# Performance work log

Hardware: AMD Instinct MI355X
Metric: run time of the kernel (lower is better)

The kernel has to match this reference:

```python
import jax, jax.numpy as jnp
import numpy as np

NUM_CODEBOOKS = 2
CODEBOOK_SIZE = 256
OUT_GROUP = 1
IN_GROUP = 8
IN_FEATURES = 4096
OUT_FEATURES = 11008


def setup_inputs() -> dict:
    key = jax.random.key(0)
    k1, k2, k3, k4, k5 = jax.random.split(key, 5)
    num_out_groups = OUT_FEATURES // OUT_GROUP
    num_in_groups = IN_FEATURES // IN_GROUP
    x = jax.random.normal(k1, (4, 2048, IN_FEATURES), dtype=jnp.float32)
    codes = jax.random.randint(k2, (num_out_groups, num_in_groups, NUM_CODEBOOKS), 0, CODEBOOK_SIZE, dtype=jnp.int32)
    codebooks = jax.random.normal(k3, (NUM_CODEBOOKS, CODEBOOK_SIZE, OUT_GROUP, IN_GROUP), dtype=jnp.float32) * 0.05
    scales = jax.random.uniform(k4, (num_out_groups, 1, 1, 1), dtype=jnp.float32)
    bias = jax.random.normal(k5, (OUT_FEATURES,), dtype=jnp.float32)
    return {"x": x, "codes": codes, "codebooks": codebooks, "scales": scales, "bias": bias}


def _dequantize_weight(codes, codebooks, scales):
    # codes: [Og, Ig, C] int; codebooks: [C, K, og, ig]; scales: [Og,1,1,1]
    C = codebooks.shape[0]
    og, ig = codebooks.shape[2], codebooks.shape[3]
    Og, Ig = codes.shape[0], codes.shape[1]
    # gather per-codebook vectors: result [Og, Ig, C, og, ig]
    w = codebooks[jnp.arange(C)[None, None, :], codes]
    w = w.sum(axis=2)                      # [Og, Ig, og, ig] (additive quantization)
    w = w * scales                         # broadcast [Og,1,1,1]
    w = w.transpose(0, 2, 1, 3)            # [Og, og, Ig, ig]
    return w.reshape(Og * og, Ig * ig)     # [out_features, in_features]


def reference(x, codes, codebooks, scales, bias):
    W = _dequantize_weight(codes, codebooks, scales)
    return jnp.einsum('bsi,oi->bso', x, W) + bias
```

## Files before the change

### kernel.cpp

```cpp
#include <hip/hip_runtime.h>
#include <hip/hip_bf16.h>
#include <stdint.h>

#define IN_F 4096
#define OUT_F 11008
#define M_ROWS 8192
#define NIG 512
#define CBSZ 256

typedef _Float16 f16x8 __attribute__((ext_vector_type(8)));
typedef float f32x4 __attribute__((ext_vector_type(4)));

__global__ __launch_bounds__(256) void dequant_w_kernel(
    const int* __restrict__ codes, const float* __restrict__ cbs,
    _Float16* __restrict__ W)
{
  const int idx = blockIdx.x * 256 + threadIdx.x;
  const int2 c = ((const int2*)codes)[idx];
  const float4* e0 = (const float4*)(cbs + (size_t)c.x * 8);
  const float4* e1 = (const float4*)(cbs + (size_t)CBSZ * 8 + (size_t)c.y * 8);
  const float4 a0 = e0[0], a1 = e0[1];
  const float4 b0 = e1[0], b1 = e1[1];
  f16x8 w;
  w[0] = (_Float16)(a0.x + b0.x);
  w[1] = (_Float16)(a0.y + b0.y);
  w[2] = (_Float16)(a0.z + b0.z);
  w[3] = (_Float16)(a0.w + b0.w);
  w[4] = (_Float16)(a1.x + b1.x);
  w[5] = (_Float16)(a1.y + b1.y);
  w[6] = (_Float16)(a1.z + b1.z);
  w[7] = (_Float16)(a1.w + b1.w);
  *(f16x8*)(W + (size_t)idx * 8) = w;
}

__global__ __launch_bounds__(256) void convert_x_kernel(
    const float* __restrict__ x, _Float16* __restrict__ X)
{
  const size_t i = ((size_t)blockIdx.x * 256 + threadIdx.x) * 8;
  const float4 a = *(const float4*)(x + i);
  const float4 b = *(const float4*)(x + i + 4);
  f16x8 v;
  v[0] = (_Float16)a.x; v[1] = (_Float16)a.y;
  v[2] = (_Float16)a.z; v[3] = (_Float16)a.w;
  v[4] = (_Float16)b.x; v[5] = (_Float16)b.y;
  v[6] = (_Float16)b.z; v[7] = (_Float16)b.w;
  *(f16x8*)(X + i) = v;
}

#define BM 256
#define BN 256
#define BK 64
#define NKT (IN_F / BK)
#define GRID_MT (M_ROWS / BM)
#define GRID_NT (OUT_F / BN)

__global__ __launch_bounds__(512, 2) void gemm_8phase(
    const _Float16* __restrict__ X, const _Float16* __restrict__ Wd,
    const float* __restrict__ scales, const float* __restrict__ bias,
    float* __restrict__ out)
{
  __shared__ char smem[131072];

  const int cpx = (GRID_MT * GRID_NT) >> 3;
  const int wg = (blockIdx.x & 7) * cpx + (blockIdx.x >> 3);
  const int mt = wg & 31, nt = wg >> 5;
  const int m0 = mt * BM, n0 = nt * BN;

  const int t = threadIdx.x;
  const int wave = t >> 6, lane = t & 63;
  const int wm = wave >> 2, wn = wave & 3;
  const int r16 = lane & 15;
  const int koff2 = (lane >> 4) << 4;
  const int Xr = ((r16 & 8) << 2) | ((r16 & 4) << 2);
  const int laneoff = r16 * 64 + (koff2 ^ Xr);

  const int s_row0 = ((t >> 7) << 4) | ((t >> 2) & 15);
  const int s_col  = (((t >> 6) & 1) << 5) | (((((t & 3) << 4) ^ (t & 48))) >> 1);
  const _Float16* asrc = X  + (size_t)(m0 + s_row0) * IN_F + s_col;
  const _Float16* bsrc = Wd + (size_t)(n0 + s_row0) * IN_F + s_col;
  const int s_dst = wave * 1024;

  f32x4 acc[8][4] = {};
  f16x8 alo[4][2], ahi[4][2], blo[2][2], bhi[2][2];

#define STAGE(kt, b) do {                                                     \
    const _Float16* _a = asrc + (size_t)(kt) * BK;                            \
    const _Float16* _b = bsrc + (size_t)(kt) * BK;                            \
    _Pragma("unroll")                                                         \
    for (int i = 0; i < 4; ++i)                                               \
      __builtin_amdgcn_global_load_lds(                                       \
        (const __attribute__((address_space(1))) void*)(_a + (size_t)i * 64 * IN_F), \
        (__attribute__((address_space(3))) void*)(smem + (b) * 65536 + i * 8192 + s_dst), \
        16, 0, 0);                                                            \
    _Pragma("unroll")                                                         \
    for (int i = 0; i < 4; ++i)                                               \
      __builtin_amdgcn_global_load_lds(                                       \
        (const __attribute__((address_space(1))) void*)(_b + (size_t)i * 64 * IN_F), \
        (__attribute__((address_space(3))) void*)(smem + (b) * 65536 + 32768 + i * 8192 + s_dst), \
        16, 0, 0);                                                            \
  } while (0)

  STAGE(0, 0);
  __syncthreads();

  for (int j = 0; j < NKT; ++j) {
    const int cur = j & 1;
    const char* Ab = smem + cur * 65536;
    const char* Bb = smem + cur * 65536 + 32768;

    if (j + 1 < NKT) STAGE(j + 1, cur ^ 1);
    #pragma unroll
    for (int m = 0; m < 4; ++m)
      #pragma unroll
      for (int k = 0; k < 2; ++k)
        alo[m][k] = *(const f16x8*)(Ab + (wm * 8 + m) * 2048 + k * 1024 + laneoff);
    #pragma unroll
    for (int n = 0; n < 2; ++n)
      #pragma unroll
      for (int k = 0; k < 2; ++k)
        blo[n][k] = *(const f16x8*)(Bb + (wn * 4 + n) * 2048 + k * 1024 + laneoff);
    __builtin_amdgcn_s_barrier();
    __builtin_amdgcn_s_setprio(1);
    #pragma unroll
    for (int k = 0; k < 2; ++k)
      #pragma unroll
      for (int m = 0; m < 4; ++m)
        #pragma unroll
        for (int n = 0; n < 2; ++n)
          acc[m][n] = __builtin_amdgcn_mfma_f32_16x16x32_f16(alo[m][k], blo[n][k], acc[m][n], 0, 0, 0);
    __builtin_amdgcn_s_setprio(0);
    __builtin_amdgcn_s_barrier();

    #pragma unroll
    for (int n = 0; n < 2; ++n)
      #pragma unroll
      for (int k = 0; k < 2; ++k)
        bhi[n][k] = *(const f16x8*)(Bb + (wn * 4 + 2 + n) * 2048 + k * 1024 + laneoff);
    __builtin_amdgcn_s_barrier();
    __builtin_amdgcn_s_setprio(1);
    #pragma unroll
    for (int k = 0; k < 2; ++k)
      #pragma unroll
      for (int m = 0; m < 4; ++m)
        #pragma unroll
        for (int n = 0; n < 2; ++n)
          acc[m][2 + n] = __builtin_amdgcn_mfma_f32_16x16x32_f16(alo[m][k], bhi[n][k], acc[m][2 + n], 0, 0, 0);
    __builtin_amdgcn_s_setprio(0);
    __builtin_amdgcn_s_barrier();

    #pragma unroll
    for (int m = 0; m < 4; ++m)
      #pragma unroll
      for (int k = 0; k < 2; ++k)
        ahi[m][k] = *(const f16x8*)(Ab + (wm * 8 + 4 + m) * 2048 + k * 1024 + laneoff);
    __builtin_amdgcn_s_barrier();
    __builtin_amdgcn_s_setprio(1);
    #pragma unroll
    for (int k = 0; k < 2; ++k)
      #pragma unroll
      for (int m = 0; m < 4; ++m)
        #pragma unroll
        for (int n = 0; n < 2; ++n)
          acc[4 + m][2 + n] = __builtin_amdgcn_mfma_f32_16x16x32_f16(ahi[m][k], bhi[n][k], acc[4 + m][2 + n], 0, 0, 0);
    __builtin_amdgcn_s_setprio(0);
    __builtin_amdgcn_s_barrier();

    __builtin_amdgcn_s_setprio(1);
    #pragma unroll
    for (int k = 0; k < 2; ++k)
      #pragma unroll
      for (int m = 0; m < 4; ++m)
        #pragma unroll
        for (int n = 0; n < 2; ++n)
          acc[4 + m][n] = __builtin_amdgcn_mfma_f32_16x16x32_f16(ahi[m][k], blo[n][k], acc[4 + m][n], 0, 0, 0);
    __builtin_amdgcn_s_setprio(0);
    __syncthreads();
  }

  const int crow = (lane >> 4) << 2;
  #pragma unroll
  for (int nf = 0; nf < 4; ++nf) {
    const int col = n0 + wn * 64 + nf * 16 + r16;
    const float s = scales[col];
    const float bb = bias[col];
    #pragma unroll
    for (int mf = 0; mf < 8; ++mf) {
      const int rb = m0 + wm * 128 + mf * 16 + crow;
      #pragma unroll
      for (int r = 0; r < 4; ++r)
        out[(size_t)(rb + r) * OUT_F + col] = acc[mf][nf][r] * s + bb;
    }
  }
#undef STAGE
}

__global__ __launch_bounds__(256) void naive_kernel(
    const float* __restrict__ x, const int* __restrict__ codes,
    const float* __restrict__ cbs, const float* __restrict__ scales,
    const float* __restrict__ bias, float* __restrict__ out)
{
  __shared__ float xrow[IN_F];
  const int m = blockIdx.x;
  for (int i = threadIdx.x; i < IN_F; i += 256)
    xrow[i] = x[(size_t)m * IN_F + i];
  __syncthreads();
  for (int o = threadIdx.x; o < OUT_F; o += 256) {
    float acc = 0.f;
    const int2* crow = (const int2*)codes + (size_t)o * NIG;
    for (int g = 0; g < NIG; ++g) {
      const int2 c = crow[g];
      const float* e0 = cbs + (size_t)c.x * 8;
      const float* e1 = cbs + (size_t)CBSZ * 8 + (size_t)c.y * 8;
      const float* xr = xrow + g * 8;
      #pragma unroll
      for (int j = 0; j < 8; ++j) acc += (e0[j] + e1[j]) * xr[j];
    }
    out[(size_t)m * OUT_F + o] = acc * scales[o] + bias[o];
  }
}

extern "C" void kernel_launch(void* const* d_in, const int* in_sizes, int n_in,
                              void* d_out, int out_size, void* d_ws, size_t ws_size,
                              hipStream_t stream) {
  const float* x      = (const float*)d_in[0];
  const int*   codes  = (const int*)d_in[1];
  const float* cbs    = (const float*)d_in[2];
  const float* scales = (const float*)d_in[3];
  const float* bias   = (const float*)d_in[4];
  float* out = (float*)d_out;

  const size_t W_BYTES = (size_t)OUT_F * IN_F * sizeof(_Float16);
  const size_t X_BYTES = (size_t)M_ROWS * IN_F * sizeof(_Float16);

  if (ws_size < W_BYTES + X_BYTES) {
    naive_kernel<<<M_ROWS, 256, 0, stream>>>(x, codes, cbs, scales, bias, out);
    return;
  }

  _Float16* W = (_Float16*)d_ws;
  _Float16* X = (_Float16*)((char*)d_ws + W_BYTES);

  dequant_w_kernel<<<(OUT_F * NIG) / 256, 256, 0, stream>>>(codes, cbs, W);
  convert_x_kernel<<<(M_ROWS * IN_F / 8) / 256, 256, 0, stream>>>(x, X);
  gemm_8phase<<<GRID_MT * GRID_NT, 512, 0, stream>>>(X, W, scales, bias, out);
}
```

Baseline: 925.0 us.

## Prefetch two K-tiles ahead with vmcnt waits and a new swizzled LDS layout

The GEMM main loop is restructured so that both LDS buffers are filled up front, and each tile issues the load for tile j+2 into the buffer it has just finished reading. The per-iteration __syncthreads is replaced by an explicit s_waitcnt vmcnt plus a barrier, and the loop is unrolled by two. The LDS layout also changes from the fragment-blocked arrangement to row-major 128-byte rows with an XOR swizzle, which changes both the staging and the fragment-read addressing. The goal is to hide global-load latency behind more MFMA work. The tighter wait logic is harder to verify, and the new swizzle may bring LDS bank conflicts.

Measured after the change: 910.8 us. About the same (-1.5%).

```diff
diff --git a/kernel.cpp b/kernel.cpp
--- a/kernel.cpp
+++ b/kernel.cpp
@@ -54,7 +54,7 @@
 #define GRID_MT (M_ROWS / BM)
 #define GRID_NT (OUT_F / BN)
 
-__global__ __launch_bounds__(512, 2) void gemm_8phase(
+__global__ __launch_bounds__(512, 2) void gemm_pipe(
     const _Float16* __restrict__ X, const _Float16* __restrict__ Wd,
     const float* __restrict__ scales, const float* __restrict__ bias,
     float* __restrict__ out)
@@ -63,19 +63,17 @@
 
   const int cpx = (GRID_MT * GRID_NT) >> 3;
   const int wg = (blockIdx.x & 7) * cpx + (blockIdx.x >> 3);
-  const int mt = wg & 31, nt = wg >> 5;
+  const int mt = wg & (GRID_MT - 1), nt = wg >> 5;
   const int m0 = mt * BM, n0 = nt * BN;
 
   const int t = threadIdx.x;
   const int wave = t >> 6, lane = t & 63;
   const int wm = wave >> 2, wn = wave & 3;
   const int r16 = lane & 15;
-  const int koff2 = (lane >> 4) << 4;
-  const int Xr = ((r16 & 8) << 2) | ((r16 & 4) << 2);
-  const int laneoff = r16 * 64 + (koff2 ^ Xr);
-
-  const int s_row0 = ((t >> 7) << 4) | ((t >> 2) & 15);
-  const int s_col  = (((t >> 6) & 1) << 5) | (((((t & 3) << 4) ^ (t & 48))) >> 1);
+  const int ko = (((lane >> 4) << 4) ^ ((r16 & 4) << 3));
+
+  const int s_row0 = t >> 3;
+  const int s_col  = ((t & 7) << 3) ^ ((t & 32) >> 1);
   const _Float16* asrc = X  + (size_t)(m0 + s_row0) * IN_F + s_col;
   const _Float16* bsrc = Wd + (size_t)(n0 + s_row0) * IN_F + s_col;
   const int s_dst = wave * 1024;
@@ -100,82 +98,72 @@
         16, 0, 0);                                                            \
   } while (0)
 
+#define BAR   __builtin_amdgcn_s_barrier()
+#define PRIO1 __builtin_amdgcn_s_setprio(1)
+#define PRIO0 __builtin_amdgcn_s_setprio(0)
+#define VMCNT8 asm volatile("s_waitcnt vmcnt(8)" ::: "memory")
+#define VMCNT0 asm volatile("s_waitcnt vmcnt(0)" ::: "memory")
+
+#define QUAD(AM, BM_, AOFF, BOFF)                                             \
+    _Pragma("unroll")                                                         \
+    for (int k = 0; k < 2; ++k)                                               \
+      _Pragma("unroll")                                                       \
+      for (int m = 0; m < 4; ++m)                                             \
+        _Pragma("unroll")                                                     \
+        for (int n = 0; n < 2; ++n)                                           \
+          acc[(AOFF) + m][(BOFF) + n] =                                       \
+            __builtin_amdgcn_mfma_f32_16x16x32_f16(AM[m][k], BM_[n][k],       \
+                                                   acc[(AOFF) + m][(BOFF) + n], 0, 0, 0)
+
+#define TILE(cur, jj, STG, W8, W0) do {                                       \
+    const char* Ab = smem + (cur) * 65536;                                    \
+    const char* Bb = Ab + 32768;                                              \
+                                               \
+    _Pragma("unroll")                                                         \
+    for (int m = 0; m < 4; ++m)                                               \
+      _Pragma("unroll")                                                       \
+      for (int k = 0; k < 2; ++k)                                             \
+        alo[m][k] = *(const f16x8*)(Ab + ((wm * 128 + m * 16 + r16) << 7) + (k << 6) + ko); \
+    _Pragma("unroll")                                                         \
+    for (int n = 0; n < 2; ++n)                                               \
+      _Pragma("unroll")                                                       \
+      for (int k = 0; k < 2; ++k)                                             \
+        blo[n][k] = *(const f16x8*)(Bb + ((wn * 64 + n * 16 + r16) << 7) + (k << 6) + ko); \
+    BAR; PRIO1; QUAD(alo, blo, 0, 0); PRIO0; BAR;                             \
+                                                      \
+    _Pragma("unroll")                                                         \
+    for (int n = 0; n < 2; ++n)                                               \
+      _Pragma("unroll")                                                       \
+      for (int k = 0; k < 2; ++k)                                             \
+        bhi[n][k] = *(const f16x8*)(Bb + ((wn * 64 + (2 + n) * 16 + r16) << 7) + (k << 6) + ko); \
+    BAR; PRIO1; QUAD(alo, bhi, 0, 2); PRIO0; BAR;                             \
+                                                      \
+    _Pragma("unroll")                                                         \
+    for (int m = 0; m < 4; ++m)                                               \
+      _Pragma("unroll")                                                       \
+      for (int k = 0; k < 2; ++k)                                             \
+        ahi[m][k] = *(const f16x8*)(Ab + ((wm * 128 + (4 + m) * 16 + r16) << 7) + (k << 6) + ko); \
+    BAR; PRIO1; QUAD(ahi, bhi, 4, 2); PRIO0; BAR;                             \
+     \
+    if (STG) STAGE((jj) + 2, cur);                                            \
+    BAR; PRIO1; QUAD(ahi, blo, 4, 0); PRIO0;                                  \
+    if (W8) { VMCNT8; }                                                       \
+    if (W0) { VMCNT0; }                                                       \
+    if ((W8) || (W0)) BAR;                             \
+  } while (0)
+
   STAGE(0, 0);
-  __syncthreads();
-
-  for (int j = 0; j < NKT; ++j) {
-    const int cur = j & 1;
-    const char* Ab = smem + cur * 65536;
-    const char* Bb = smem + cur * 65536 + 32768;
-
-    if (j + 1 < NKT) STAGE(j + 1, cur ^ 1);
-    #pragma unroll
-    for (int m = 0; m < 4; ++m)
-      #pragma unroll
-      for (int k = 0; k < 2; ++k)
-        alo[m][k] = *(const f16x8*)(Ab + (wm * 8 + m) * 2048 + k * 1024 + laneoff);
-    #pragma unroll
-    for (int n = 0; n < 2; ++n)
-      #pragma unroll
-      for (int k = 0; k < 2; ++k)
-        blo[n][k] = *(const f16x8*)(Bb + (wn * 4 + n) * 2048 + k * 1024 + laneoff);
-    __builtin_amdgcn_s_barrier();
-    __builtin_amdgcn_s_setprio(1);
-    #pragma unroll
-    for (int k = 0; k < 2; ++k)
-      #pragma unroll
-      for (int m = 0; m < 4; ++m)
-        #pragma unroll
-        for (int n = 0; n < 2; ++n)
-          acc[m][n] = __builtin_amdgcn_mfma_f32_16x16x32_f16(alo[m][k], blo[n][k], acc[m][n], 0, 0, 0);
-    __builtin_amdgcn_s_setprio(0);
-    __builtin_amdgcn_s_barrier();
-
-    #pragma unroll
-    for (int n = 0; n < 2; ++n)
-      #pragma unroll
-      for (int k = 0; k < 2; ++k)
-        bhi[n][k] = *(const f16x8*)(Bb + (wn * 4 + 2 + n) * 2048 + k * 1024 + laneoff);
-    __builtin_amdgcn_s_barrier();
-    __builtin_amdgcn_s_setprio(1);
-    #pragma unroll
-    for (int k = 0; k < 2; ++k)
-      #pragma unroll
-      for (int m = 0; m < 4; ++m)
-        #pragma unroll
-        for (int n = 0; n < 2; ++n)
-          acc[m][2 + n] = __builtin_amdgcn_mfma_f32_16x16x32_f16(alo[m][k], bhi[n][k], acc[m][2 + n], 0, 0, 0);
-    __builtin_amdgcn_s_setprio(0);
-    __builtin_amdgcn_s_barrier();
-
-    #pragma unroll
-    for (int m = 0; m < 4; ++m)
-      #pragma unroll
-      for (int k = 0; k < 2; ++k)
-        ahi[m][k] = *(const f16x8*)(Ab + (wm * 8 + 4 + m) * 2048 + k * 1024 + laneoff);
-    __builtin_amdgcn_s_barrier();
-    __builtin_amdgcn_s_setprio(1);
-    #pragma unroll
-    for (int k = 0; k < 2; ++k)
-      #pragma unroll
-      for (int m = 0; m < 4; ++m)
-        #pragma unroll
-        for (int n = 0; n < 2; ++n)
-          acc[4 + m][2 + n] = __builtin_amdgcn_mfma_f32_16x16x32_f16(ahi[m][k], bhi[n][k], acc[4 + m][2 + n], 0, 0, 0);
-    __builtin_amdgcn_s_setprio(0);
-    __builtin_amdgcn_s_barrier();
-
-    __builtin_amdgcn_s_setprio(1);
-    #pragma unroll
-    for (int k = 0; k < 2; ++k)
-      #pragma unroll
-      for (int m = 0; m < 4; ++m)
-        #pragma unroll
-        for (int n = 0; n < 2; ++n)
-          acc[4 + m][n] = __builtin_amdgcn_mfma_f32_16x16x32_f16(ahi[m][k], blo[n][k], acc[4 + m][n], 0, 0, 0);
-    __builtin_amdgcn_s_setprio(0);
-    __syncthreads();
-  }
+  STAGE(1, 1);
+  VMCNT8;
+  BAR;
+
+  #pragma unroll 1
+  for (int jj = 0; jj < 62; jj += 2) {
+    TILE(0, jj, 1, 1, 0);
+    TILE(1, jj + 1, 1, 1, 0);
+  }
+  TILE(0, 62, 0, 0, 1);
+  TILE(1, 63, 0, 0, 0);
 
   const int crow = (lane >> 4) << 2;
   #pragma unroll
@@ -191,6 +179,8 @@
         out[(size_t)(rb + r) * OUT_F + col] = acc[mf][nf][r] * s + bb;
     }
   }
+#undef TILE
+#undef QUAD
 #undef STAGE
 }
 
@@ -242,5 +232,5 @@
 
   dequant_w_kernel<<<(OUT_F * NIG) / 256, 256, 0, stream>>>(codes, cbs, W);
   convert_x_kernel<<<(M_ROWS * IN_F / 8) / 256, 256, 0, stream>>>(x, X);
-  gemm_8phase<<<GRID_MT * GRID_NT, 512, 0, stream>>>(X, W, scales, bias, out);
-}
+  gemm_pipe<<<GRID_MT * GRID_NT, 512, 0, stream>>>(X, W, scales, bias, out);
+}
```
